# Performance work log

Hardware: AMD Instinct MI355X
Metric: run time of the kernel (lower is better)

## Reference

```python
import jax, jax.numpy as jnp
import numpy as np

BATCH = 4
N_PER = 300          # queries per image (equal split -> cum_feats_batch = [0,300,600,900,1200])
NUM_FEATS = BATCH * N_PER
IN_DIM = 256
KEY_DIM = 32
FH = FW = 160


def setup_inputs() -> dict:
    key = jax.random.key(0)
    ks = jax.random.split(key, 6)
    return {
        "in_feats": jax.random.normal(ks[0], (NUM_FEATS, IN_DIM), dtype=jnp.float32),
        "feat_map": jax.random.normal(ks[1], (BATCH, IN_DIM, FH, FW), dtype=jnp.float32),
        "qry_w": jax.random.normal(ks[2], (KEY_DIM, IN_DIM), dtype=jnp.float32) * 0.05,
        "qry_b": jax.random.normal(ks[3], (KEY_DIM,), dtype=jnp.float32) * 0.05,
        "key_w": jax.random.normal(ks[4], (KEY_DIM, IN_DIM), dtype=jnp.float32) * 0.05,
        "key_b": jax.random.normal(ks[5], (KEY_DIM,), dtype=jnp.float32) * 0.05,
    }


def reference(in_feats, feat_map, qry_w, qry_b, key_w, key_b):
    # qry module: Linear projecting input features -> dynamic conv weights  [NF, C]
    qry_feats = in_feats @ qry_w.T + qry_b
    # key module: 1x1 conv on the first feature map  [B, C, H, W]
    key_map = jnp.einsum('oc,bchw->bohw', key_w, feat_map) + key_b[None, :, None, None]
    # per-batch dynamic 1x1 conv: F.conv2d(key_map[i:i+1], qry_feats[i0:i1,:,None,None])
    # with an equal split of queries per image this is a batched einsum.
    q = qry_feats.reshape(BATCH, N_PER, KEY_DIM)            # [B, N, C]
    seg_logits = jnp.einsum('bnc,bchw->bnhw', q, key_map)   # [B, N, H, W]
    return seg_logits.reshape(NUM_FEATS, FH, FW)            # [num_feats, fH, fW]
```

## Files before the change

kernel.cpp:

```cpp
#include <hip/hip_runtime.h>
#include <hip/hip_bf16.h>

#define BATCH 4
#define N_PER 300
#define IN_DIM 256
#define KEY_DIM 32
#define FH 160
#define FW 160
#define HW (FH * FW)
#define NQ (BATCH * N_PER)
#define Q_ELEMS (NQ * KEY_DIM)
#define KWT_ELEMS (IN_DIM * KEY_DIM)
#define PREP_TOTAL (Q_ELEMS + KWT_ELEMS)

__global__ __launch_bounds__(256) void prep_kernel(
        const float* __restrict__ in_feats,
        const float* __restrict__ qry_w,
        const float* __restrict__ qry_b,
        const float* __restrict__ key_w,
        float* __restrict__ ws) {
    int gid = blockIdx.x * 256 + threadIdx.x;
    if (gid < Q_ELEMS) {
        int n = gid >> 5;
        int c = gid & 31;
        const float* __restrict__ fr = in_feats + n * IN_DIM;
        const float* __restrict__ wr = qry_w + c * IN_DIM;
        float a0 = qry_b[c], a1 = 0.f, a2 = 0.f, a3 = 0.f;
        #pragma unroll 4
        for (int k = 0; k < IN_DIM; k += 4) {
            a0 += fr[k + 0] * wr[k + 0];
            a1 += fr[k + 1] * wr[k + 1];
            a2 += fr[k + 2] * wr[k + 2];
            a3 += fr[k + 3] * wr[k + 3];
        }
        ws[gid] = (a0 + a1) + (a2 + a3);
    } else {
        int i = gid - Q_ELEMS;
        int c = i >> 5;
        int o = i & 31;
        ws[gid] = key_w[o * IN_DIM + c];
    }
}

__global__ __launch_bounds__(256) void main_kernel(
        const float* __restrict__ feat_map,
        const float* __restrict__ key_b,
        const float* __restrict__ ws,
        float* __restrict__ out) {
    const int b = blockIdx.y;
    const int p = blockIdx.x * 256 + threadIdx.x;

    const float* __restrict__ fb  = feat_map + ((size_t)b * IN_DIM) * HW + p;
    const float* __restrict__ kwT = ws + Q_ELEMS;

    float key[KEY_DIM];
    #pragma unroll
    for (int o = 0; o < KEY_DIM; ++o) key[o] = key_b[o];

    #pragma unroll 8
    for (int c = 0; c < IN_DIM; ++c) {
        float f = fb[(size_t)c * HW];
        const float* __restrict__ kr = kwT + c * KEY_DIM;
        #pragma unroll
        for (int o = 0; o < KEY_DIM; ++o)
            key[o] += kr[o] * f;
    }

    const float* __restrict__ qb = ws + (size_t)b * N_PER * KEY_DIM;
    float* __restrict__ ob = out + ((size_t)b * N_PER) * HW + p;
    for (int n = 0; n < N_PER; ++n) {
        const float* __restrict__ qn = qb + n * KEY_DIM;
        float a0 = 0.f, a1 = 0.f, a2 = 0.f, a3 = 0.f;
        #pragma unroll
        for (int c = 0; c < KEY_DIM; c += 4) {
            a0 += qn[c + 0] * key[c + 0];
            a1 += qn[c + 1] * key[c + 1];
            a2 += qn[c + 2] * key[c + 2];
            a3 += qn[c + 3] * key[c + 3];
        }
        ob[(size_t)n * HW] = (a0 + a1) + (a2 + a3);
    }
}

extern "C" void kernel_launch(void* const* d_in, const int* in_sizes, int n_in,
                              void* d_out, int out_size, void* d_ws, size_t ws_size,
                              hipStream_t stream) {
    const float* in_feats = (const float*)d_in[0];
    const float* feat_map = (const float*)d_in[1];
    const float* qry_w    = (const float*)d_in[2];
    const float* qry_b    = (const float*)d_in[3];
    const float* key_w    = (const float*)d_in[4];
    const float* key_b    = (const float*)d_in[5];
    float* ws  = (float*)d_ws;
    float* out = (float*)d_out;

    prep_kernel<<<dim3(PREP_TOTAL / 256), dim3(256), 0, stream>>>(
        in_feats, qry_w, qry_b, key_w, ws);

    dim3 grid(HW / 256, BATCH);
    main_kernel<<<grid, dim3(256), 0, stream>>>(feat_map, key_b, ws, out);
}
```

Baseline: 282.1 us.

## Split channel reduction across four warp groups and partition query outputs per group

```diff
diff --git a/kernel.cpp b/kernel.cpp
--- a/kernel.cpp
+++ b/kernel.cpp
@@ -1,5 +1,4 @@
 #include <hip/hip_runtime.h>
-#include <hip/hip_bf16.h>
 
 #define BATCH 4
 #define N_PER 300
@@ -11,7 +10,10 @@
 #define NQ (BATCH * N_PER)
 #define Q_ELEMS (NQ * KEY_DIM)
 #define KWT_ELEMS (IN_DIM * KEY_DIM)
-#define PREP_TOTAL (Q_ELEMS + KWT_ELEMS)
+
+#define QBLOCKS NQ
+#define TBLOCKS (KWT_ELEMS / 256)
+#define NCHUNK (N_PER / 4)
 
 __global__ __launch_bounds__(256) void prep_kernel(
         const float* __restrict__ in_feats,
@@ -19,64 +21,99 @@
         const float* __restrict__ qry_b,
         const float* __restrict__ key_w,
         float* __restrict__ ws) {
-    int gid = blockIdx.x * 256 + threadIdx.x;
-    if (gid < Q_ELEMS) {
-        int n = gid >> 5;
-        int c = gid & 31;
-        const float* __restrict__ fr = in_feats + n * IN_DIM;
-        const float* __restrict__ wr = qry_w + c * IN_DIM;
-        float a0 = qry_b[c], a1 = 0.f, a2 = 0.f, a3 = 0.f;
-        #pragma unroll 4
-        for (int k = 0; k < IN_DIM; k += 4) {
-            a0 += fr[k + 0] * wr[k + 0];
-            a1 += fr[k + 1] * wr[k + 1];
-            a2 += fr[k + 2] * wr[k + 2];
-            a3 += fr[k + 3] * wr[k + 3];
+    const int bid = blockIdx.x;
+    const int t = threadIdx.x;
+    if (bid < QBLOCKS) {
+        const int n   = bid;
+        const int c   = t >> 3;
+        const int sub = t & 7;
+        const float4* __restrict__ f4 =
+            (const float4*)(in_feats + n * IN_DIM + sub * 32);
+        const float4* __restrict__ w4 =
+            (const float4*)(qry_w + c * IN_DIM + sub * 32);
+        float a0 = 0.f, a1 = 0.f, a2 = 0.f, a3 = 0.f;
+        #pragma unroll
+        for (int j = 0; j < 8; ++j) {
+            float4 fv = f4[j];
+            float4 wv = w4[j];
+            a0 += fv.x * wv.x;
+            a1 += fv.y * wv.y;
+            a2 += fv.z * wv.z;
+            a3 += fv.w * wv.w;
         }
-        ws[gid] = (a0 + a1) + (a2 + a3);
+        float s = (a0 + a1) + (a2 + a3);
+        s += __shfl_xor(s, 1);
+        s += __shfl_xor(s, 2);
+        s += __shfl_xor(s, 4);
+        if (sub == 0) ws[n * KEY_DIM + c] = s + qry_b[c];
     } else {
-        int i = gid - Q_ELEMS;
-        int c = i >> 5;
-        int o = i & 31;
-        ws[gid] = key_w[o * IN_DIM + c];
+        const int i = (bid - QBLOCKS) * 256 + t;
+        const int c = i >> 5;
+        const int o = i & 31;
+        ws[Q_ELEMS + i] = key_w[o * IN_DIM + c];
     }
 }
 
-__global__ __launch_bounds__(256) void main_kernel(
+__global__ __launch_bounds__(1024, 4) void main_kernel(
         const float* __restrict__ feat_map,
         const float* __restrict__ key_b,
         const float* __restrict__ ws,
         float* __restrict__ out) {
-    const int b = blockIdx.y;
-    const int p = blockIdx.x * 256 + threadIdx.x;
+    __shared__ float part[2][KEY_DIM][256];
 
-    const float* __restrict__ fb  = feat_map + ((size_t)b * IN_DIM) * HW + p;
-    const float* __restrict__ kwT = ws + Q_ELEMS;
+    const int t   = threadIdx.x;
+    const int p   = t & 255;
+    const int g   = t >> 8;
+    const int b   = blockIdx.y;
+    const int pix = blockIdx.x * 256 + p;
+
+    const float* __restrict__ fb  =
+        feat_map + ((size_t)b * IN_DIM + g * 64) * HW + pix;
+    const float* __restrict__ kwT = ws + Q_ELEMS + (g * 64) * KEY_DIM;
+
+    float acc[KEY_DIM];
+    #pragma unroll
+    for (int o = 0; o < KEY_DIM; ++o) acc[o] = 0.f;
+
+    #pragma unroll 8
+    for (int c = 0; c < 64; ++c) {
+        float f = fb[(size_t)c * HW];
+        const float* __restrict__ kr = kwT + c * KEY_DIM;
+        #pragma unroll
+        for (int o = 0; o < KEY_DIM; ++o) acc[o] += kr[o] * f;
+    }
+
+    if (g < 2) {
+        #pragma unroll
+        for (int o = 0; o < KEY_DIM; ++o) part[g][o][p] = acc[o];
+    }
+    __syncthreads();
+    if (g >= 2) {
+        #pragma unroll
+        for (int o = 0; o < KEY_DIM; ++o) part[g - 2][o][p] += acc[o];
+    }
+    __syncthreads();
 
     float key[KEY_DIM];
     #pragma unroll
-    for (int o = 0; o < KEY_DIM; ++o) key[o] = key_b[o];
+    for (int o = 0; o < KEY_DIM; ++o)
+        key[o] = part[0][o][p] + part[1][o][p] + key_b[o];
 
-    #pragma unroll 8
-    for (int c = 0; c < IN_DIM; ++c) {
-        float f = fb[(size_t)c * HW];
-        const float* __restrict__ kr = kwT + c * KEY_DIM;
-        #pragma unroll
-        for (int o = 0; o < KEY_DIM; ++o)
-            key[o] += kr[o] * f;
-    }
+    const int ng = __builtin_amdgcn_readfirstlane(g);
+    const float* __restrict__ qb =
+        ws + ((size_t)b * N_PER + ng * NCHUNK) * KEY_DIM;
+    float* __restrict__ ob =
+        out + ((size_t)b * N_PER + (size_t)ng * NCHUNK) * HW + pix;
 
-    const float* __restrict__ qb = ws + (size_t)b * N_PER * KEY_DIM;
-    float* __restrict__ ob = out + ((size_t)b * N_PER) * HW + p;
-    for (int n = 0; n < N_PER; ++n) {
+    for (int n = 0; n < NCHUNK; ++n) {
         const float* __restrict__ qn = qb + n * KEY_DIM;
         float a0 = 0.f, a1 = 0.f, a2 = 0.f, a3 = 0.f;
         #pragma unroll
-        for (int c = 0; c < KEY_DIM; c += 4) {
-            a0 += qn[c + 0] * key[c + 0];
-            a1 += qn[c + 1] * key[c + 1];
-            a2 += qn[c + 2] * key[c + 2];
-            a3 += qn[c + 3] * key[c + 3];
+        for (int c2 = 0; c2 < KEY_DIM; c2 += 4) {
+            a0 += qn[c2 + 0] * key[c2 + 0];
+            a1 += qn[c2 + 1] * key[c2 + 1];
+            a2 += qn[c2 + 2] * key[c2 + 2];
+            a3 += qn[c2 + 3] * key[c2 + 3];
         }
         ob[(size_t)n * HW] = (a0 + a1) + (a2 + a3);
     }
@@ -94,9 +131,9 @@
     float* ws  = (float*)d_ws;
     float* out = (float*)d_out;
 
-    prep_kernel<<<dim3(PREP_TOTAL / 256), dim3(256), 0, stream>>>(
+    prep_kernel<<<dim3(QBLOCKS + TBLOCKS), dim3(256), 0, stream>>>(
         in_feats, qry_w, qry_b, key_w, ws);
 
-    dim3 grid(HW / 256, BATCH);
-    main_kernel<<<grid, dim3(256), 0, stream>>>(feat_map, key_b, ws, out);
+    main_kernel<<<dim3(HW / 256, BATCH), dim3(1024), 0, stream>>>(
+        feat_map, key_b, ws, out);
 }
```

Result: slower. 451.7 us (+60.1%).
